# Kernel tuning notes

Measured on AMD Instinct MI355X. Metric: run time of the kernel, lower is better.

## Reference

```python
import jax, jax.numpy as jnp
import numpy as np

EMBED_DIM = 768
NUM_HEADS = 12
D_K = EMBED_DIM // NUM_HEADS
FFN_DIM = 3072
N_QUBITS = 8
LN_EPS = 1e-5


def layer_norm(x, g, b):
    mu = jnp.mean(x, axis=-1, keepdims=True)
    var = jnp.mean(jnp.square(x - mu), axis=-1, keepdims=True)
    return (x - mu) * jax.lax.rsqrt(var + LN_EPS) * g + b


def setup_inputs() -> dict:
    key = jax.random.key(0)
    ks = jax.random.split(key, 8)
    B, S = 4, 2048
    s_comb = 1.0 / np.sqrt(EMBED_DIM)
    s_w1 = 1.0 / np.sqrt(N_QUBITS)
    s_w2 = 1.0 / np.sqrt(FFN_DIM)
    return {
        "x": jax.random.normal(ks[0], (B, S, EMBED_DIM), jnp.float32),
        "combine_w": jax.random.uniform(ks[1], (EMBED_DIM, EMBED_DIM), jnp.float32, -s_comb, s_comb),
        "theta": jax.random.normal(ks[2], (N_QUBITS,), jnp.float32),
        "w1": jax.random.uniform(ks[3], (FFN_DIM, N_QUBITS), jnp.float32, -s_w1, s_w1),
        "w2": jax.random.uniform(ks[4], (EMBED_DIM, FFN_DIM), jnp.float32, -s_w2, s_w2),
        "ln1_g": jnp.ones((EMBED_DIM,), jnp.float32),
        "ln1_b": jnp.zeros((EMBED_DIM,), jnp.float32),
        "ln2_g": jnp.ones((EMBED_DIM,), jnp.float32),
        "ln2_b": jnp.zeros((EMBED_DIM,), jnp.float32),
    }


def reference(x, combine_w, theta, w1, w2, ln1_g, ln1_b, ln2_g, ln2_b):
    B, S, D = x.shape
    # --- attention (q = k = v = x split into heads; QLayer is never used in forward) ---
    xh = x.reshape(B, S, NUM_HEADS, D_K).transpose(0, 2, 1, 3)  # [B,H,S,dk]
    scores = jnp.einsum("bhqd,bhkd->bhqk", xh, xh) / jnp.sqrt(jnp.asarray(D_K, x.dtype))
    probs = jax.nn.softmax(scores, axis=-1)
    attn = jnp.einsum("bhqk,bhkd->bhqd", probs, xh)
    attn = attn.transpose(0, 2, 1, 3).reshape(B, S, D)
    attn_out = attn @ combine_w.T
    # --- residual + norm1 ---
    h = layer_norm(x + attn_out, ln1_g, ln1_b)
    # --- quantum FFN: RX(x_i) then RY(theta_i) per wire, <Z_i> = cos(x_i)*cos(theta_i) ---
    meas = jnp.cos(h[..., :N_QUBITS]) * jnp.cos(theta)  # [B,S,nq]
    ffn = jax.nn.relu(meas @ w1.T) @ w2.T               # [B,S,D]
    # --- residual + norm2 ---
    return layer_norm(h + ffn, ln2_g, ln2_b)
```

## Files before the change

### kernel.cpp

```cpp
#include <hip/hip_runtime.h>
#include <math.h>


#define B_    4
#define S_    2048
#define D_    768
#define H_    12
#define DK_   64
#define FFN_  3072
#define NQ_   8
#define M_    (B_ * S_)

#define AS1 __attribute__((address_space(1)))
#define AS3 __attribute__((address_space(3)))

typedef __attribute__((ext_vector_type(8))) short bf16x8;
typedef __attribute__((ext_vector_type(4))) float f32x4;

static __device__ __forceinline__ unsigned short f2bf(float f) {
    unsigned u = __float_as_uint(f);
    unsigned r = (u + 0x7FFFu + ((u >> 16) & 1u)) >> 16;
    return (unsigned short)r;
}
static __device__ __forceinline__ float bf2f(unsigned short h) {
    return __uint_as_float((unsigned)h << 16);
}
static __device__ __forceinline__ bf16x8 pack8(float4 a, float4 b) {
    bf16x8 r;
    r[0] = (short)f2bf(a.x); r[1] = (short)f2bf(a.y);
    r[2] = (short)f2bf(a.z); r[3] = (short)f2bf(a.w);
    r[4] = (short)f2bf(b.x); r[5] = (short)f2bf(b.y);
    r[6] = (short)f2bf(b.z); r[7] = (short)f2bf(b.w);
    return r;
}

#define XCH  786432
#define CWCH 73728
#define W2CH 294912
__global__ void convert_all(const float* __restrict__ x, const float* __restrict__ cw,
                            const float* __restrict__ w2,
                            unsigned short* __restrict__ xb, unsigned short* __restrict__ cwb,
                            unsigned short* __restrict__ w2b)
{
    int idx = blockIdx.x * 256 + threadIdx.x;
    const float* src; unsigned short* dst; int c;
    if (idx < XCH)              { src = x;  dst = xb;  c = idx; }
    else if (idx < XCH + CWCH)  { src = cw; dst = cwb; c = idx - XCH; }
    else { c = idx - XCH - CWCH; if (c >= W2CH) return; src = w2; dst = w2b; }
    float4 f0 = *reinterpret_cast<const float4*>(src + (size_t)c * 8);
    float4 f1 = *reinterpret_cast<const float4*>(src + (size_t)c * 8 + 4);
    *reinterpret_cast<bf16x8*>(dst + (size_t)c * 8) = pack8(f0, f1);
}

__global__ __launch_bounds__(256, 2)
void attn_mfma(const unsigned short* __restrict__ xb, unsigned short* __restrict__ attnb)
{
    __shared__ __align__(16) short    Ks[2][128 * 64];
    __shared__ __align__(16) unsigned Vt32[64 * 64];
    __shared__ __align__(16) short    Ps[4][32 * 128];

    const int tid = threadIdx.x;
    const int w   = tid >> 6;
    const int l   = tid & 63;
    const int g   = l >> 4;
    const int l15 = l & 15;

    const int flat = blockIdx.x;
    const int rx = flat & 7;
    const int t  = flat >> 3;
    const int gq = t & 15;
    const int G  = (t >> 4) * 8 + rx;
    const int hh = G % 12, bb = G / 12;
    const int q0 = gq * 128;

    const unsigned short* xh = xb + ((size_t)bb * S_) * D_ + hh * DK_;

    bf16x8 qf[2][2];
    {
        const unsigned short* xq = xh + (size_t)(q0 + w * 32) * D_;
        #pragma unroll
        for (int qt = 0; qt < 2; ++qt)
            #pragma unroll
            for (int ks = 0; ks < 2; ++ks)
                qf[qt][ks] = *reinterpret_cast<const bf16x8*>(
                    xq + (size_t)(qt * 16 + l15) * D_ + ks * 32 + g * 8);
    }

    f32x4 oacc[2][4];
    float lsum[2][4];
    #pragma unroll
    for (int qt = 0; qt < 2; ++qt)
        #pragma unroll
        for (int i = 0; i < 4; ++i) {
            oacc[qt][i] = (f32x4){0.f, 0.f, 0.f, 0.f};
            lsum[qt][i] = 0.f;
        }

    short* Pw = Ps[w];
    bf16x8 vh0, vh1, vh2, vh3;
    const int kvp = tid & 63, dg = tid >> 6;

    auto stageK = [&](int kt, int buf) {
        const unsigned short* xk = xh + (size_t)(kt * 128) * D_;
        #pragma unroll
        for (int it = 0; it < 4; ++it) {
            int c = tid + it * 256;
            int r = c >> 3, b2 = c & 7;
            const unsigned short* gsrc = xk + (size_t)r * D_ + ((b2 ^ (r & 7)) << 3);
            __builtin_amdgcn_global_load_lds(
                (const AS1 void*)gsrc,
                (AS3 void*)(&Ks[buf][0] + ((it * 256 + w * 64) << 3)), 16, 0, 0);
        }
    };
    auto loadV = [&](int kt) {
        const unsigned short* ra = xh + (size_t)(kt * 128 + 2 * kvp) * D_ + dg * 16;
        vh0 = *reinterpret_cast<const bf16x8*>(ra);
        vh1 = *reinterpret_cast<const bf16x8*>(ra + 8);
        vh2 = *reinterpret_cast<const bf16x8*>(ra + D_);
        vh3 = *reinterpret_cast<const bf16x8*>(ra + D_ + 8);
    };
    auto writeV = [&]() {
        #pragma unroll
        for (int j = 0; j < 8; ++j) {
            int d0 = dg * 16 + j;
            Vt32[d0 * 64 + (kvp ^ ((d0 & 7) << 2))] =
                (unsigned)(unsigned short)vh0[j] | ((unsigned)(unsigned short)vh2[j] << 16);
            int d1 = dg * 16 + 8 + j;
            Vt32[d1 * 64 + (kvp ^ ((d1 & 7) << 2))] =
                (unsigned)(unsigned short)vh1[j] | ((unsigned)(unsigned short)vh3[j] << 16);
        }
    };

    stageK(0, 0);
    loadV(0);
    writeV();
    __syncthreads();

    for (int kt = 0; kt < S_ / 128; ++kt) {
        const int cur = kt & 1;
        if (kt < S_ / 128 - 1) {
            stageK(kt + 1, cur ^ 1);
            loadV(kt + 1);
        }

        f32x4 sacc[2][8];
        #pragma unroll
        for (int qt = 0; qt < 2; ++qt)
            #pragma unroll
            for (int kj = 0; kj < 8; ++kj) sacc[qt][kj] = (f32x4){0.f, 0.f, 0.f, 0.f};

        #pragma unroll
        for (int ks = 0; ks < 2; ++ks) {
            bf16x8 kf[8];
            #pragma unroll
            for (int kj = 0; kj < 8; ++kj) {
                int r = kj * 16 + l15;
                kf[kj] = *reinterpret_cast<const bf16x8*>(
                    &Ks[cur][r * 64 + (((ks * 4 + g) ^ (r & 7)) << 3)]);
            }
            #pragma unroll
            for (int qt = 0; qt < 2; ++qt)
                #pragma unroll
                for (int kj = 0; kj < 8; ++kj)
                    sacc[qt][kj] = __builtin_amdgcn_mfma_f32_16x16x32_bf16(
                        qf[qt][ks], kf[kj], sacc[qt][kj], 0, 0, 0);
        }

        #pragma unroll
        for (int qt = 0; qt < 2; ++qt) {
            #pragma unroll
            for (int reg = 0; reg < 4; ++reg) {
                int q = qt * 16 + g * 4 + reg;
                short* pr = Pw + q * 128;
                int qs = q & 7;
                float psum = 0.f;
                #pragma unroll
                for (int kj = 0; kj < 8; ++kj) {
                    float p = exp2f(sacc[qt][kj][reg] * 0.18033688f);
                    psum += p;
                    int c = kj * 16 + l15;
                    pr[(((c >> 3) ^ qs) << 3) | (c & 7)] =
                        (short)((__float_as_uint(p) + 0x8000u) >> 16);
                }
                lsum[qt][reg] += psum;
            }
        }

        #pragma unroll
        for (int ks = 0; ks < 4; ++ks) {
            bf16x8 pf[2], vf[4];
            #pragma unroll
            for (int qt = 0; qt < 2; ++qt) {
                int q = qt * 16 + l15;
                pf[qt] = *reinterpret_cast<const bf16x8*>(
                    &Pw[q * 128 + (((ks * 4 + g) ^ (q & 7)) << 3)]);
            }
            #pragma unroll
            for (int dt = 0; dt < 4; ++dt) {
                int d = dt * 16 + l15;
                vf[dt] = *reinterpret_cast<const bf16x8*>(
                    &Vt32[d * 64 + ((ks * 16 + g * 4) ^ ((d & 7) << 2))]);
            }
            #pragma unroll
            for (int qt = 0; qt < 2; ++qt)
                #pragma unroll
                for (int dt = 0; dt < 4; ++dt)
                    oacc[qt][dt] = __builtin_amdgcn_mfma_f32_16x16x32_bf16(
                        pf[qt], vf[dt], oacc[qt][dt], 0, 0, 0);
        }

        __syncthreads();
        if (kt < S_ / 128 - 1) writeV();
        __syncthreads();
    }

    unsigned short* ao = attnb + ((size_t)bb * S_ + q0 + w * 32) * D_ + hh * DK_;
    #pragma unroll
    for (int qt = 0; qt < 2; ++qt)
        #pragma unroll
        for (int reg = 0; reg < 4; ++reg) {
            float s = lsum[qt][reg];
            s += __shfl_xor(s, 1); s += __shfl_xor(s, 2);
            s += __shfl_xor(s, 4); s += __shfl_xor(s, 8);
            float inv = 1.0f / s;
            int q = qt * 16 + g * 4 + reg;
            unsigned short* rp = ao + (size_t)q * D_;
            #pragma unroll
            for (int dt = 0; dt < 4; ++dt)
                rp[dt * 16 + l15] = f2bf(oacc[qt][dt][reg] * inv);
        }
}

template<int KDIM>
__global__ __launch_bounds__(256, 3)
void gemm_bf16(const unsigned short* __restrict__ A, const unsigned short* __restrict__ Bw,
               const float* __restrict__ res, float* __restrict__ out)
{
    __shared__ __align__(16) short As[64 * 64];
    __shared__ __align__(16) short Bs[128 * 64];

    const int tid = threadIdx.x;
    const int w = tid >> 6, l = tid & 63, g = l >> 4, l15 = l & 15;
    const int wr = w >> 1, wc = w & 1;
    const int m0 = blockIdx.x * 64, n0 = blockIdx.y * 128;

    f32x4 acc[2][4];
    #pragma unroll
    for (int i = 0; i < 2; ++i)
        #pragma unroll
        for (int j = 0; j < 4; ++j) acc[i][j] = (f32x4){0.f, 0.f, 0.f, 0.f};

    for (int k0 = 0; k0 < KDIM; k0 += 64) {
        __syncthreads();
        #pragma unroll
        for (int it = 0; it < 2; ++it) {
            int c = tid + it * 256;
            int r = c >> 3, b = c & 7;
            const unsigned short* ga = A + (size_t)(m0 + r) * KDIM + k0 + ((b ^ (r & 7)) << 3);
            __builtin_amdgcn_global_load_lds((const AS1 void*)ga,
                (AS3 void*)(As + ((it * 256 + w * 64) << 3)), 16, 0, 0);
        }
        #pragma unroll
        for (int it = 0; it < 4; ++it) {
            int c = tid + it * 256;
            int r = c >> 3, b = c & 7;
            const unsigned short* gb = Bw + (size_t)(n0 + r) * KDIM + k0 + ((b ^ (r & 7)) << 3);
            __builtin_amdgcn_global_load_lds((const AS1 void*)gb,
                (AS3 void*)(Bs + ((it * 256 + w * 64) << 3)), 16, 0, 0);
        }
        __syncthreads();

        #pragma unroll
        for (int ks = 0; ks < 2; ++ks) {
            bf16x8 af[2], bf[4];
            #pragma unroll
            for (int mt = 0; mt < 2; ++mt) {
                int r = wr * 32 + mt * 16 + l15;
                af[mt] = *reinterpret_cast<const bf16x8*>(
                    &As[r * 64 + (((ks * 4 + g) ^ (r & 7)) << 3)]);
            }
            #pragma unroll
            for (int nt = 0; nt < 4; ++nt) {
                int cc = wc * 64 + nt * 16 + l15;
                bf[nt] = *reinterpret_cast<const bf16x8*>(
                    &Bs[cc * 64 + (((ks * 4 + g) ^ (cc & 7)) << 3)]);
            }
            #pragma unroll
            for (int mt = 0; mt < 2; ++mt)
                #pragma unroll
                for (int nt = 0; nt < 4; ++nt)
                    acc[mt][nt] = __builtin_amdgcn_mfma_f32_16x16x32_bf16(
                        af[mt], bf[nt], acc[mt][nt], 0, 0, 0);
        }
    }

    #pragma unroll
    for (int mt = 0; mt < 2; ++mt)
        #pragma unroll
        for (int reg = 0; reg < 4; ++reg) {
            size_t row = (size_t)m0 + wr * 32 + mt * 16 + g * 4 + reg;
            #pragma unroll
            for (int nt = 0; nt < 4; ++nt) {
                int col = n0 + wc * 64 + nt * 16 + l15;
                out[row * D_ + col] = acc[mt][nt][reg] + res[row * D_ + col];
            }
        }
}

__global__ __launch_bounds__(256, 2)
void tbuild(const float* __restrict__ h, const float* __restrict__ theta,
            const float* __restrict__ w1, unsigned short* __restrict__ Tb)
{
    __shared__ __align__(16) short w1s[FFN_ * NQ_];

    const int tid = threadIdx.x;
    const int w = tid >> 6, l = tid & 63;

    #pragma unroll
    for (int it = 0; it < 12; ++it) {
        int c = tid + it * 256;
        float4 f0 = *reinterpret_cast<const float4*>(w1 + (size_t)c * 8);
        float4 f1 = *reinterpret_cast<const float4*>(w1 + (size_t)c * 8 + 4);
        *reinterpret_cast<bf16x8*>(&w1s[(c ^ ((c >> 3) & 7)) * 8]) = pack8(f0, f1);
    }
    __syncthreads();

    float cth[NQ_];
    #pragma unroll
    for (int q = 0; q < NQ_; ++q) cth[q] = cosf(theta[q]);

    #pragma unroll
    for (int rr = 0; rr < 4; ++rr) {
        int row = blockIdx.x * 16 + w * 4 + rr;
        const float* hp = h + (size_t)row * D_;
        float meas[NQ_];
        #pragma unroll
        for (int q = 0; q < NQ_; ++q) meas[q] = cosf(hp[q]) * cth[q];
        unsigned short* outp = Tb + (size_t)row * FFN_;
        #pragma unroll
        for (int itc = 0; itc < 6; ++itc) {
            int cbase = itc * 512 + l * 8;
            bf16x8 tv;
            #pragma unroll
            for (int cc = 0; cc < 8; ++cc) {
                bf16x8 wv = *reinterpret_cast<const bf16x8*>(
                    &w1s[((cbase + cc) ^ (l & 7)) * 8]);
                float t = 0.f;
                #pragma unroll
                for (int q = 0; q < NQ_; ++q)
                    t = fmaf(meas[q], bf2f((unsigned short)wv[q]), t);
                tv[cc] = (short)f2bf(fmaxf(t, 0.f));
            }
            *reinterpret_cast<bf16x8*>(&outp[cbase]) = tv;
        }
    }
}

__global__ __launch_bounds__(256, 4)
void ln_kernel(const float* __restrict__ in, const float* __restrict__ g,
               const float* __restrict__ bt, float* __restrict__ out)
{
    const int wave = threadIdx.x >> 6, lane = threadIdx.x & 63;
    const size_t row = (size_t)blockIdx.x * 4 + wave;
    const float* p = in + row * D_;
    float v[12];
    float sum = 0.f;
    #pragma unroll
    for (int c = 0; c < 3; ++c) {
        float4 f = *reinterpret_cast<const float4*>(p + (c * 64 + lane) * 4);
        v[c*4+0] = f.x; v[c*4+1] = f.y; v[c*4+2] = f.z; v[c*4+3] = f.w;
        sum += (f.x + f.y) + (f.z + f.w);
    }
    #pragma unroll
    for (int msk = 1; msk < 64; msk <<= 1) sum += __shfl_xor(sum, msk);
    const float mu = sum * (1.0f / 768.0f);
    float vs = 0.f;
    #pragma unroll
    for (int k = 0; k < 12; ++k) { float d = v[k] - mu; vs = fmaf(d, d, vs); }
    #pragma unroll
    for (int msk = 1; msk < 64; msk <<= 1) vs += __shfl_xor(vs, msk);
    const float rstd = rsqrtf(vs * (1.0f / 768.0f) + 1e-5f);
    float* po = out + row * D_;
    #pragma unroll
    for (int c = 0; c < 3; ++c) {
        const int base = (c * 64 + lane) * 4;
        float4 gg = *reinterpret_cast<const float4*>(g + base);
        float4 bb2 = *reinterpret_cast<const float4*>(bt + base);
        float4 r;
        r.x = (v[c*4+0] - mu) * rstd * gg.x + bb2.x;
        r.y = (v[c*4+1] - mu) * rstd * gg.y + bb2.y;
        r.z = (v[c*4+2] - mu) * rstd * gg.z + bb2.z;
        r.w = (v[c*4+3] - mu) * rstd * gg.w + bb2.w;
        *reinterpret_cast<float4*>(po + base) = r;
    }
}

extern "C" void kernel_launch(void* const* d_in, const int* in_sizes, int n_in,
                              void* d_out, int out_size, void* d_ws, size_t ws_size,
                              hipStream_t stream)
{
    const float* x   = (const float*)d_in[0];
    const float* cw  = (const float*)d_in[1];
    const float* th  = (const float*)d_in[2];
    const float* w1  = (const float*)d_in[3];
    const float* w2  = (const float*)d_in[4];
    const float* g1  = (const float*)d_in[5];
    const float* b1  = (const float*)d_in[6];
    const float* g2  = (const float*)d_in[7];
    const float* b2  = (const float*)d_in[8];
    float* out = (float*)d_out;

    const size_t HB  = 25165824;
    const size_t TBB = 50331648;
    const size_t CWB = 1179648;

    char* wsc = (char*)d_ws;
    unsigned short* xbuf  = (unsigned short*)wsc;
    float*          hbuf  = (float*)wsc;
    unsigned short* attnb = (unsigned short*)(wsc + HB);
    unsigned short* Tb    = (unsigned short*)(wsc + HB);
    unsigned short* cwb   = (unsigned short*)(wsc + HB + TBB);
    unsigned short* w2b   = (unsigned short*)(wsc + HB + TBB + CWB);

    convert_all    <<<dim3((XCH + CWCH + W2CH) / 256), 256, 0, stream>>>(x, cw, w2, xbuf, cwb, w2b);
    attn_mfma      <<<dim3(16 * H_ * B_), 256, 0, stream>>>(xbuf, attnb);
    gemm_bf16<D_>  <<<dim3(M_ / 64, D_ / 128), 256, 0, stream>>>(attnb, cwb, x, out);
    ln_kernel      <<<dim3(M_ / 4), 256, 0, stream>>>(out, g1, b1, hbuf);
    tbuild         <<<dim3(M_ / 16), 256, 0, stream>>>(hbuf, th, w1, Tb);
    gemm_bf16<FFN_><<<dim3(M_ / 64, D_ / 128), 256, 0, stream>>>(Tb, w2b, hbuf, out);
    ln_kernel      <<<dim3(M_ / 4), 256, 0, stream>>>(out, g2, b2, out);
}
```

Measured before the change: 541.2 us.

## Rework attention LDS staging for occupancy and double-buffer GEMM tiles

The attention kernel drops its double-buffered K tile in LDS and instead prefetches K into registers, writing it to a single LDS buffer after each iteration. It also processes the 128-key tile in two halves so the P scratch is halved, and raises the launch bound to three blocks per CU. The output is now staged through LDS so global stores are coalesced 16-byte writes. Separately, the GEMM kernel gains double-buffered A/B tiles so the next K-slab loads overlap the MFMAs. The costs are more registers held for prefetch and more LDS in the GEMM, which may reduce its occupancy.

After: 672.6 us. 24.3% more time.

```diff
diff --git a/kernel.cpp b/kernel.cpp
--- a/kernel.cpp
+++ b/kernel.cpp
@@ -52,12 +52,12 @@
     *reinterpret_cast<bf16x8*>(dst + (size_t)c * 8) = pack8(f0, f1);
 }
 
-__global__ __launch_bounds__(256, 2)
+__global__ __launch_bounds__(256, 3)
 void attn_mfma(const unsigned short* __restrict__ xb, unsigned short* __restrict__ attnb)
 {
-    __shared__ __align__(16) short    Ks[2][128 * 64];
+    __shared__ __align__(16) short    Ks[128 * 64];
     __shared__ __align__(16) unsigned Vt32[64 * 64];
-    __shared__ __align__(16) short    Ps[4][32 * 128];
+    __shared__ __align__(16) short    Ps[4][32 * 64];
 
     const int tid = threadIdx.x;
     const int w   = tid >> 6;
@@ -97,124 +97,125 @@
         }
 
     short* Pw = Ps[w];
-    bf16x8 vh0, vh1, vh2, vh3;
-    const int kvp = tid & 63, dg = tid >> 6;
-
-    auto stageK = [&](int kt, int buf) {
+    bf16x8 kreg0, kreg1, kreg2, kreg3;
+    bf16x8 vreg0, vreg1, vreg2, vreg3;
+
+    auto loadK = [&](int kt) {
         const unsigned short* xk = xh + (size_t)(kt * 128) * D_;
-        #pragma unroll
-        for (int it = 0; it < 4; ++it) {
-            int c = tid + it * 256;
-            int r = c >> 3, b2 = c & 7;
-            const unsigned short* gsrc = xk + (size_t)r * D_ + ((b2 ^ (r & 7)) << 3);
-            __builtin_amdgcn_global_load_lds(
-                (const AS1 void*)gsrc,
-                (AS3 void*)(&Ks[buf][0] + ((it * 256 + w * 64) << 3)), 16, 0, 0);
-        }
+        int c0 = tid, c1 = tid + 256, c2 = tid + 512, c3 = tid + 768;
+        kreg0 = *reinterpret_cast<const bf16x8*>(xk + (size_t)(c0 >> 3) * D_ + (c0 & 7) * 8);
+        kreg1 = *reinterpret_cast<const bf16x8*>(xk + (size_t)(c1 >> 3) * D_ + (c1 & 7) * 8);
+        kreg2 = *reinterpret_cast<const bf16x8*>(xk + (size_t)(c2 >> 3) * D_ + (c2 & 7) * 8);
+        kreg3 = *reinterpret_cast<const bf16x8*>(xk + (size_t)(c3 >> 3) * D_ + (c3 & 7) * 8);
+    };
+    auto writeK = [&]() {
+        int c0 = tid, c1 = tid + 256, c2 = tid + 512, c3 = tid + 768;
+        #define WRK(cc, rg) { int r = (cc) >> 3, b2 = (cc) & 7; \
+            *reinterpret_cast<bf16x8*>(&Ks[r * 64 + ((b2 ^ (r & 7)) << 3)]) = rg; }
+        WRK(c0, kreg0) WRK(c1, kreg1) WRK(c2, kreg2) WRK(c3, kreg3)
+        #undef WRK
     };
     auto loadV = [&](int kt) {
-        const unsigned short* ra = xh + (size_t)(kt * 128 + 2 * kvp) * D_ + dg * 16;
-        vh0 = *reinterpret_cast<const bf16x8*>(ra);
-        vh1 = *reinterpret_cast<const bf16x8*>(ra + 8);
-        vh2 = *reinterpret_cast<const bf16x8*>(ra + D_);
-        vh3 = *reinterpret_cast<const bf16x8*>(ra + D_ + 8);
+        const unsigned short* ra = xh + (size_t)(kt * 128 + 2 * l) * D_ + w * 16;
+        vreg0 = *reinterpret_cast<const bf16x8*>(ra);
+        vreg1 = *reinterpret_cast<const bf16x8*>(ra + 8);
+        vreg2 = *reinterpret_cast<const bf16x8*>(ra + D_);
+        vreg3 = *reinterpret_cast<const bf16x8*>(ra + D_ + 8);
     };
     auto writeV = [&]() {
         #pragma unroll
         for (int j = 0; j < 8; ++j) {
-            int d0 = dg * 16 + j;
-            Vt32[d0 * 64 + (kvp ^ ((d0 & 7) << 2))] =
-                (unsigned)(unsigned short)vh0[j] | ((unsigned)(unsigned short)vh2[j] << 16);
-            int d1 = dg * 16 + 8 + j;
-            Vt32[d1 * 64 + (kvp ^ ((d1 & 7) << 2))] =
-                (unsigned)(unsigned short)vh1[j] | ((unsigned)(unsigned short)vh3[j] << 16);
+            int d0 = w * 16 + j;
+            Vt32[d0 * 64 + (l ^ ((d0 & 7) << 2))] =
+                (unsigned)(unsigned short)vreg0[j] | ((unsigned)(unsigned short)vreg2[j] << 16);
+            int d1 = w * 16 + 8 + j;
+            Vt32[d1 * 64 + (l ^ ((d1 & 7) << 2))] =
+                (unsigned)(unsigned short)vreg1[j] | ((unsigned)(unsigned short)vreg3[j] << 16);
         }
     };
 
-    stageK(0, 0);
-    loadV(0);
-    writeV();
+    loadK(0); loadV(0);
+    writeK(); writeV();
     __syncthreads();
 
     for (int kt = 0; kt < S_ / 128; ++kt) {
-        const int cur = kt & 1;
-        if (kt < S_ / 128 - 1) {
-            stageK(kt + 1, cur ^ 1);
-            loadV(kt + 1);
-        }
-
-        f32x4 sacc[2][8];
-        #pragma unroll
-        for (int qt = 0; qt < 2; ++qt)
-            #pragma unroll
-            for (int kj = 0; kj < 8; ++kj) sacc[qt][kj] = (f32x4){0.f, 0.f, 0.f, 0.f};
-
-        #pragma unroll
-        for (int ks = 0; ks < 2; ++ks) {
-            bf16x8 kf[8];
-            #pragma unroll
-            for (int kj = 0; kj < 8; ++kj) {
-                int r = kj * 16 + l15;
-                kf[kj] = *reinterpret_cast<const bf16x8*>(
-                    &Ks[cur][r * 64 + (((ks * 4 + g) ^ (r & 7)) << 3)]);
-            }
+        if (kt < S_ / 128 - 1) { loadK(kt + 1); loadV(kt + 1); }
+
+        #pragma unroll
+        for (int h = 0; h < 2; ++h) {
+            f32x4 sacc[2][4];
             #pragma unroll
             for (int qt = 0; qt < 2; ++qt)
                 #pragma unroll
-                for (int kj = 0; kj < 8; ++kj)
-                    sacc[qt][kj] = __builtin_amdgcn_mfma_f32_16x16x32_bf16(
-                        qf[qt][ks], kf[kj], sacc[qt][kj], 0, 0, 0);
-        }
-
-        #pragma unroll
-        for (int qt = 0; qt < 2; ++qt) {
-            #pragma unroll
-            for (int reg = 0; reg < 4; ++reg) {
-                int q = qt * 16 + g * 4 + reg;
-                short* pr = Pw + q * 128;
-                int qs = q & 7;
-                float psum = 0.f;
-                #pragma unroll
-                for (int kj = 0; kj < 8; ++kj) {
-                    float p = exp2f(sacc[qt][kj][reg] * 0.18033688f);
-                    psum += p;
-                    int c = kj * 16 + l15;
-                    pr[(((c >> 3) ^ qs) << 3) | (c & 7)] =
-                        (short)((__float_as_uint(p) + 0x8000u) >> 16);
+                for (int kj = 0; kj < 4; ++kj) sacc[qt][kj] = (f32x4){0.f, 0.f, 0.f, 0.f};
+
+            #pragma unroll
+            for (int ks = 0; ks < 2; ++ks) {
+                bf16x8 kf[4];
+                #pragma unroll
+                for (int kj = 0; kj < 4; ++kj) {
+                    int r = (h * 4 + kj) * 16 + l15;
+                    kf[kj] = *reinterpret_cast<const bf16x8*>(
+                        &Ks[r * 64 + (((ks * 4 + g) ^ (r & 7)) << 3)]);
                 }
-                lsum[qt][reg] += psum;
-            }
-        }
-
-        #pragma unroll
-        for (int ks = 0; ks < 4; ++ks) {
-            bf16x8 pf[2], vf[4];
+                #pragma unroll
+                for (int qt = 0; qt < 2; ++qt)
+                    #pragma unroll
+                    for (int kj = 0; kj < 4; ++kj)
+                        sacc[qt][kj] = __builtin_amdgcn_mfma_f32_16x16x32_bf16(
+                            qf[qt][ks], kf[kj], sacc[qt][kj], 0, 0, 0);
+            }
+
             #pragma unroll
             for (int qt = 0; qt < 2; ++qt) {
-                int q = qt * 16 + l15;
-                pf[qt] = *reinterpret_cast<const bf16x8*>(
-                    &Pw[q * 128 + (((ks * 4 + g) ^ (q & 7)) << 3)]);
-            }
-            #pragma unroll
-            for (int dt = 0; dt < 4; ++dt) {
-                int d = dt * 16 + l15;
-                vf[dt] = *reinterpret_cast<const bf16x8*>(
-                    &Vt32[d * 64 + ((ks * 16 + g * 4) ^ ((d & 7) << 2))]);
-            }
-            #pragma unroll
-            for (int qt = 0; qt < 2; ++qt)
-                #pragma unroll
-                for (int dt = 0; dt < 4; ++dt)
-                    oacc[qt][dt] = __builtin_amdgcn_mfma_f32_16x16x32_bf16(
-                        pf[qt], vf[dt], oacc[qt][dt], 0, 0, 0);
+                #pragma unroll
+                for (int reg = 0; reg < 4; ++reg) {
+                    int q = qt * 16 + g * 4 + reg;
+                    short* pr = Pw + q * 64;
+                    int qs = q & 7;
+                    float psum = 0.f;
+                    #pragma unroll
+                    for (int kj = 0; kj < 4; ++kj) {
+                        float p = exp2f(sacc[qt][kj][reg] * 0.18033688f);
+                        psum += p;
+                        int c = kj * 16 + l15;
+                        pr[(((c >> 3) ^ qs) << 3) | (c & 7)] =
+                            (short)((__float_as_uint(p) + 0x8000u) >> 16);
+                    }
+                    lsum[qt][reg] += psum;
+                }
+            }
+
+            #pragma unroll
+            for (int s = 0; s < 2; ++s) {
+                int kse = h * 2 + s;
+                bf16x8 pf[2], vf[4];
+                #pragma unroll
+                for (int qt = 0; qt < 2; ++qt) {
+                    int q = qt * 16 + l15;
+                    pf[qt] = *reinterpret_cast<const bf16x8*>(
+                        &Pw[q * 64 + (((s * 4 + g) ^ (q & 7)) << 3)]);
+                }
+                #pragma unroll
+                for (int dt = 0; dt < 4; ++dt) {
+                    int d = dt * 16 + l15;
+                    vf[dt] = *reinterpret_cast<const bf16x8*>(
+                        &Vt32[d * 64 + ((kse * 16 + g * 4) ^ ((d & 7) << 2))]);
+                }
+                #pragma unroll
+                for (int qt = 0; qt < 2; ++qt)
+                    #pragma unroll
+                    for (int dt = 0; dt < 4; ++dt)
+                        oacc[qt][dt] = __builtin_amdgcn_mfma_f32_16x16x32_bf16(
+                            pf[qt], vf[dt], oacc[qt][dt], 0, 0, 0);
+            }
         }
 
         __syncthreads();
-        if (kt < S_ / 128 - 1) writeV();
+        if (kt < S_ / 128 - 1) { writeK(); writeV(); }
         __syncthreads();
     }
 
-    unsigned short* ao = attnb + ((size_t)bb * S_ + q0 + w * 32) * D_ + hh * DK_;
     #pragma unroll
     for (int qt = 0; qt < 2; ++qt)
         #pragma unroll
@@ -224,11 +225,23 @@
             s += __shfl_xor(s, 4); s += __shfl_xor(s, 8);
             float inv = 1.0f / s;
             int q = qt * 16 + g * 4 + reg;
-            unsigned short* rp = ao + (size_t)q * D_;
-            #pragma unroll
-            for (int dt = 0; dt < 4; ++dt)
-                rp[dt * 16 + l15] = f2bf(oacc[qt][dt][reg] * inv);
-        }
+            int qs = q & 7;
+            #pragma unroll
+            for (int dt = 0; dt < 4; ++dt) {
+                int d = dt * 16 + l15;
+                Pw[q * 64 + ((((d >> 3) ^ qs) << 3) | (d & 7))] =
+                    (short)f2bf(oacc[qt][dt][reg] * inv);
+            }
+        }
+    unsigned short* ao = attnb + ((size_t)bb * S_ + q0 + w * 32) * D_ + hh * DK_;
+    #pragma unroll
+    for (int i = 0; i < 4; ++i) {
+        int idx = l + i * 64;
+        int rr = idx >> 3, cc = idx & 7;
+        bf16x8 vv = *reinterpret_cast<const bf16x8*>(
+            &Pw[rr * 64 + ((cc ^ (rr & 7)) << 3)]);
+        *reinterpret_cast<bf16x8*>(ao + (size_t)rr * D_ + cc * 8) = vv;
+    }
 }
 
 template<int KDIM>
@@ -236,29 +249,22 @@
 void gemm_bf16(const unsigned short* __restrict__ A, const unsigned short* __restrict__ Bw,
                const float* __restrict__ res, float* __restrict__ out)
 {
-    __shared__ __align__(16) short As[64 * 64];
-    __shared__ __align__(16) short Bs[128 * 64];
+    __shared__ __align__(16) short As[2][64 * 64];
+    __shared__ __align__(16) short Bs[2][128 * 64];
 
     const int tid = threadIdx.x;
     const int w = tid >> 6, l = tid & 63, g = l >> 4, l15 = l & 15;
     const int wr = w >> 1, wc = w & 1;
     const int m0 = blockIdx.x * 64, n0 = blockIdx.y * 128;
 
-    f32x4 acc[2][4];
-    #pragma unroll
-    for (int i = 0; i < 2; ++i)
-        #pragma unroll
-        for (int j = 0; j < 4; ++j) acc[i][j] = (f32x4){0.f, 0.f, 0.f, 0.f};
-
-    for (int k0 = 0; k0 < KDIM; k0 += 64) {
-        __syncthreads();
+    auto stage = [&](int k0, int buf) {
         #pragma unroll
         for (int it = 0; it < 2; ++it) {
             int c = tid + it * 256;
             int r = c >> 3, b = c & 7;
             const unsigned short* ga = A + (size_t)(m0 + r) * KDIM + k0 + ((b ^ (r & 7)) << 3);
             __builtin_amdgcn_global_load_lds((const AS1 void*)ga,
-                (AS3 void*)(As + ((it * 256 + w * 64) << 3)), 16, 0, 0);
+                (AS3 void*)(&As[buf][0] + ((it * 256 + w * 64) << 3)), 16, 0, 0);
         }
         #pragma unroll
         for (int it = 0; it < 4; ++it) {
@@ -266,9 +272,23 @@
             int r = c >> 3, b = c & 7;
             const unsigned short* gb = Bw + (size_t)(n0 + r) * KDIM + k0 + ((b ^ (r & 7)) << 3);
             __builtin_amdgcn_global_load_lds((const AS1 void*)gb,
-                (AS3 void*)(Bs + ((it * 256 + w * 64) << 3)), 16, 0, 0);
-        }
-        __syncthreads();
+                (AS3 void*)(&Bs[buf][0] + ((it * 256 + w * 64) << 3)), 16, 0, 0);
+        }
+    };
+
+    f32x4 acc[2][4];
+    #pragma unroll
+    for (int i = 0; i < 2; ++i)
+        #pragma unroll
+        for (int j = 0; j < 4; ++j) acc[i][j] = (f32x4){0.f, 0.f, 0.f, 0.f};
+
+    stage(0, 0);
+    __syncthreads();
+
+    const int NS = KDIM / 64;
+    int cur = 0;
+    for (int s = 0; s < NS; ++s) {
+        if (s + 1 < NS) stage((s + 1) * 64, cur ^ 1);
 
         #pragma unroll
         for (int ks = 0; ks < 2; ++ks) {
@@ -277,13 +297,13 @@
             for (int mt = 0; mt < 2; ++mt) {
                 int r = wr * 32 + mt * 16 + l15;
                 af[mt] = *reinterpret_cast<const bf16x8*>(
-                    &As[r * 64 + (((ks * 4 + g) ^ (r & 7)) << 3)]);
+                    &As[cur][r * 64 + (((ks * 4 + g) ^ (r & 7)) << 3)]);
             }
             #pragma unroll
             for (int nt = 0; nt < 4; ++nt) {
                 int cc = wc * 64 + nt * 16 + l15;
                 bf[nt] = *reinterpret_cast<const bf16x8*>(
-                    &Bs[cc * 64 + (((ks * 4 + g) ^ (cc & 7)) << 3)]);
+                    &Bs[cur][cc * 64 + (((ks * 4 + g) ^ (cc & 7)) << 3)]);
             }
             #pragma unroll
             for (int mt = 0; mt < 2; ++mt)
@@ -292,6 +312,9 @@
                     acc[mt][nt] = __builtin_amdgcn_mfma_f32_16x16x32_bf16(
                         af[mt], bf[nt], acc[mt][nt], 0, 0, 0);
         }
+
+        __syncthreads();
+        cur ^= 1;
     }
 
     #pragma unroll
```
